# Performance work log

Hardware: AMD Instinct MI355X
Metric: run time of the kernel (lower is better)

## Reference

```python
import jax, jax.numpy as jnp
import numpy as np

N_USERS = 100000
N_ITEMS = 50000
NNZ = 1600000
DIM = 64


def setup_inputs() -> dict:
    key = jax.random.key(0)
    k1, k2, k3, k4, k5, k6, k7 = jax.random.split(key, 7)
    user_x = jax.random.normal(k1, (N_USERS, DIM), dtype=jnp.float32)
    item_x = jax.random.normal(k2, (N_ITEMS, DIM), dtype=jnp.float32)
    # Xavier-uniform-like init for the two weight matrices
    limit = float(np.sqrt(6.0 / (DIM + DIM)))
    user_weight = jax.random.uniform(k3, (DIM, DIM), jnp.float32, -limit, limit)
    item_weight = jax.random.uniform(k4, (DIM, DIM), jnp.float32, -limit, limit)
    # Bipartite adjacency in COO form: ui_graph[r, c] = v ; iu_graph is its transpose
    ui_rows = jax.random.randint(k5, (NNZ,), 0, N_USERS, dtype=jnp.int32)
    ui_cols = jax.random.randint(k6, (NNZ,), 0, N_ITEMS, dtype=jnp.int32)
    ui_vals = jax.random.uniform(k7, (NNZ,), dtype=jnp.float32)
    return {
        "user_x": user_x,
        "item_x": item_x,
        "user_weight": user_weight,
        "item_weight": item_weight,
        "ui_rows": ui_rows,
        "ui_cols": ui_cols,
        "ui_vals": ui_vals,
    }


def _spmm(rows, cols, vals, dense, num_segments):
    # sparse[rows, cols] @ dense  -> gather source rows, scale, scatter-add to dest
    msgs = vals[:, None] * dense[cols]                      # [nnz, d]
    return jax.ops.segment_sum(msgs, rows, num_segments=num_segments)


def reference(user_x, item_x, user_weight, item_weight, ui_rows, ui_cols, ui_vals):
    # dropout p=0.0 -> identity (module default)
    xw_user = user_x @ user_weight                          # [n_users, d]
    xw_item = item_x @ item_weight                          # [n_items, d]
    # out_user = ui_graph @ xw_item ; out_item = iu_graph @ xw_user (iu = ui^T)
    out_user = _spmm(ui_rows, ui_cols, ui_vals, xw_item, N_USERS)
    out_item = _spmm(ui_cols, ui_rows, ui_vals, xw_user, N_ITEMS)
    return jax.nn.relu(out_user), jax.nn.relu(out_item)
```

## Files before the change

### kernel.cpp

```cpp
#include <hip/hip_runtime.h>
#include <hip/hip_bf16.h>

#define N_USERS 100000
#define N_ITEMS 50000
#define NNZ_EDGES 1600000
#define DIM 64

#define BSHIFT_U 7
#define BD_U 128
#define BSHIFT_I 6
#define BD_I 64
#define NBU ((N_USERS + BD_U - 1) / BD_U)
#define NBI ((N_ITEMS + BD_I - 1) / BD_I)
#define NB_MAX 782
#define TILE 4096
#define CAP 2432

#define PREP_GU ((N_USERS + 127) / 128)
#define PREP_GI ((N_ITEMS + 127) / 128)
#define PREP_BIN ((NNZ_EDGES + TILE - 1) / TILE)


__device__ inline unsigned short f32_to_bf16(float f) {
  unsigned u = __float_as_uint(f);
  unsigned r = (u + 0x7FFFu + ((u >> 16) & 1u)) >> 16;
  return (unsigned short)r;
}
__device__ inline float bf16_to_f32(unsigned short h) {
  return __uint_as_float((unsigned)h << 16);
}

__global__ __launch_bounds__(512) void prep_kernel(
    const float* __restrict__ Xu, const float* __restrict__ Wu,
    unsigned short* __restrict__ Yu,
    const float* __restrict__ Xi, const float* __restrict__ Wi,
    unsigned short* __restrict__ Yi,
    const int* __restrict__ rows, const int* __restrict__ cols,
    const float* __restrict__ vals,
    int* __restrict__ cur_u, int* __restrict__ cur_i,
    uint2* __restrict__ out_u, uint2* __restrict__ out_i) {
  __shared__ char smem[49152];
  const int tid = threadIdx.x, lane = tid & 63, wid = tid >> 6;

  if (blockIdx.x < PREP_GU + PREP_GI) {
    float* sW = (float*)smem;
    float* sXTb = (float*)(smem + 16384);
    const int sub = tid >> 8;
    const int stid = tid & 255;

    const float* X; const float* W; unsigned short* Y; int nrows, row_base;
    if (blockIdx.x < PREP_GU) {
      X = Xu; W = Wu; Y = Yu; nrows = N_USERS;
      row_base = blockIdx.x * 128 + sub * 64;
    } else {
      X = Xi; W = Wi; Y = Yi; nrows = N_ITEMS;
      row_base = (blockIdx.x - PREP_GU) * 128 + sub * 64;
    }

    {
      const float4* Wv = (const float4*)W;
      float4* sWv = (float4*)sW;
      #pragma unroll
      for (int i = 0; i < 2; ++i) sWv[tid + i * 512] = Wv[tid + i * 512];
    }
    float* sXT = sXTb + sub * 64 * 64;
    {
      const int r = stid & 63;
      const int k0 = (stid >> 6) * 16;
      const int grow = row_base + r;
      #pragma unroll
      for (int i = 0; i < 4; ++i) {
        float4 v = make_float4(0.f, 0.f, 0.f, 0.f);
        if (grow < nrows) v = ((const float4*)(X + (size_t)grow * DIM + k0))[i];
        sXT[(k0 + i * 4 + 0) * 64 + r] = v.x;
        sXT[(k0 + i * 4 + 1) * 64 + r] = v.y;
        sXT[(k0 + i * 4 + 2) * 64 + r] = v.z;
        sXT[(k0 + i * 4 + 3) * 64 + r] = v.w;
      }
    }
    __syncthreads();

    const int tx = stid & 15;
    const int ty = stid >> 4;
    float acc[4][4] = {{0.f}};

    #pragma unroll 8
    for (int k = 0; k < 64; ++k) {
      const float4 a = *(const float4*)&sXT[k * 64 + ty * 4];
      const float4 b = *(const float4*)&sW[k * 64 + tx * 4];
      acc[0][0] = fmaf(a.x, b.x, acc[0][0]);
      acc[0][1] = fmaf(a.x, b.y, acc[0][1]);
      acc[0][2] = fmaf(a.x, b.z, acc[0][2]);
      acc[0][3] = fmaf(a.x, b.w, acc[0][3]);
      acc[1][0] = fmaf(a.y, b.x, acc[1][0]);
      acc[1][1] = fmaf(a.y, b.y, acc[1][1]);
      acc[1][2] = fmaf(a.y, b.z, acc[1][2]);
      acc[1][3] = fmaf(a.y, b.w, acc[1][3]);
      acc[2][0] = fmaf(a.z, b.x, acc[2][0]);
      acc[2][1] = fmaf(a.z, b.y, acc[2][1]);
      acc[2][2] = fmaf(a.z, b.z, acc[2][2]);
      acc[2][3] = fmaf(a.z, b.w, acc[2][3]);
      acc[3][0] = fmaf(a.w, b.x, acc[3][0]);
      acc[3][1] = fmaf(a.w, b.y, acc[3][1]);
      acc[3][2] = fmaf(a.w, b.z, acc[3][2]);
      acc[3][3] = fmaf(a.w, b.w, acc[3][3]);
    }

    #pragma unroll
    for (int r = 0; r < 4; ++r) {
      const int grow = row_base + ty * 4 + r;
      if (grow < nrows) {
        ushort4 o;
        o.x = f32_to_bf16(acc[r][0]);
        o.y = f32_to_bf16(acc[r][1]);
        o.z = f32_to_bf16(acc[r][2]);
        o.w = f32_to_bf16(acc[r][3]);
        *(ushort4*)(Y + (size_t)grow * DIM + tx * 4) = o;
      }
    }
    return;
  }

  uint2* sbuf = (uint2*)smem;
  unsigned short* sbk = (unsigned short*)(smem + 32768);
  int* sh   = (int*)(smem + 40960);
  int* scnt = (int*)(smem + 44088);
  int* s_w  = (int*)(smem + 47232);

  const int tbase = (blockIdx.x - (PREP_GU + PREP_GI)) * TILE;
  const int total = min(TILE, NNZ_EDGES - tbase);

  int er[8], ec[8]; unsigned ev[8];
  #pragma unroll
  for (int k = 0; k < 8; ++k) {
    const int i = tbase + k * 512 + tid;
    if (i < NNZ_EDGES) {
      er[k] = rows[i];
      ec[k] = cols[i];
      ev[k] = __float_as_uint(vals[i]);
    } else {
      er[k] = -1; ec[k] = 0; ev[k] = 0;
    }
  }

#define BIN_PHASE(BKEXPR, PKEXPR, NB, CUR, OUT)                                \
  {                                                                            \
    for (int j = tid; j < (NB); j += 512) sh[j] = 0;                           \
    __syncthreads();                                                           \
    int bk[8]; unsigned pk[8];                                                 \
    _Pragma("unroll")                                                          \
    for (int k = 0; k < 8; ++k) {                                              \
      if (er[k] >= 0) {                                                        \
        bk[k] = (BKEXPR); pk[k] = (PKEXPR);                                    \
        atomicAdd(&sh[bk[k]], 1);                                              \
      } else { bk[k] = -1; pk[k] = 0; }                                        \
    }                                                                          \
    __syncthreads();                                                           \
    int carry = 0;                                                             \
    for (int cb = 0; cb < (NB); cb += 512) {                                   \
      const int idx = cb + tid;                                                \
      const int x = (idx < (NB)) ? sh[idx] : 0;                                \
      int incl = x;                                                            \
      _Pragma("unroll")                                                        \
      for (int d = 1; d < 64; d <<= 1) {                                       \
        int t = __shfl_up(incl, d);                                            \
        if (lane >= d) incl += t;                                              \
      }                                                                        \
      if (lane == 63) s_w[wid] = incl;                                         \
      __syncthreads();                                                         \
      if (tid == 0) {                                                          \
        int a = 0;                                                             \
        _Pragma("unroll")                                                      \
        for (int w = 0; w < 8; ++w) { const int t = s_w[w]; s_w[w] = a; a += t; } \
        s_w[8] = a;                                                            \
      }                                                                        \
      __syncthreads();                                                         \
      const int excl = carry + s_w[wid] + incl - x;                            \
      if (idx < (NB)) { scnt[idx] = x; sh[idx] = excl; }                       \
      carry += s_w[8];                                                         \
      __syncthreads();                                                         \
    }                                                                          \
    _Pragma("unroll")                                                          \
    for (int k = 0; k < 8; ++k) {                                              \
      if (bk[k] >= 0) {                                                        \
        const int p = atomicAdd(&sh[bk[k]], 1);                                \
        sbuf[p] = make_uint2(pk[k], ev[k]);                                    \
        sbk[p] = (unsigned short)bk[k];                                        \
      }                                                                        \
    }                                                                          \
    __syncthreads();                                                           \
    for (int idx = tid; idx < (NB); idx += 512) {                              \
      const int c = scnt[idx];                                                 \
      const int excl = sh[idx] - c;                                            \
      int g = 0;                                                               \
      if (c > 0) g = atomicAdd(&(CUR)[idx], c);                                \
      scnt[idx] = excl;                                                        \
      sh[idx] = idx * CAP + g;                                                 \
    }                                                                          \
    __syncthreads();                                                           \
    for (int p = tid; p < total; p += 512) {                                   \
      const int b = sbk[p];                                                    \
      (OUT)[sh[b] + (p - scnt[b])] = sbuf[p];                                  \
    }                                                                          \
    __syncthreads();                                                           \
  }

  BIN_PHASE(er[k] >> BSHIFT_U,
            ((unsigned)(er[k] & (BD_U - 1)) << 25) | ((unsigned)ec[k] << 7),
            NBU, cur_u, out_u)
  BIN_PHASE(ec[k] >> BSHIFT_I,
            ((unsigned)(ec[k] & (BD_I - 1)) << 25) | ((unsigned)er[k] << 7),
            NBI, cur_i, out_i)
#undef BIN_PHASE
}

__global__ __launch_bounds__(512) void sort_spmm_kernel(
    const uint2* __restrict__ bin_u, const int* __restrict__ cur_u,
    const unsigned short* __restrict__ xw_item, float* __restrict__ out_user,
    const uint2* __restrict__ bin_i, const int* __restrict__ cur_i,
    const unsigned short* __restrict__ xw_user, float* __restrict__ out_item) {
  __shared__ uint2 sbuf[CAP];
  __shared__ int cnt[128];
  __shared__ int roff[128];
  __shared__ int s_w[2];
  const int tid = threadIdx.x;
  const int lane = tid & 63, wid = tid >> 6;

  const uint2* bin; const int* cur; const unsigned short* xw; float* out;
  int b, bd, ndst;
  if (blockIdx.x < NBU) {
    b = blockIdx.x; bd = BD_U; ndst = N_USERS;
    bin = bin_u; cur = cur_u; xw = xw_item; out = out_user;
  } else {
    b = blockIdx.x - NBU; bd = BD_I; ndst = N_ITEMS;
    bin = bin_i; cur = cur_i; xw = xw_user; out = out_item;
  }
  const int beg = b * CAP;
  const int n = min(cur[b], CAP);

  if (tid < bd) cnt[tid] = 0;
  __syncthreads();

  uint2 rg[5];
  #pragma unroll
  for (int k = 0; k < 5; ++k) {
    const int i = k * 512 + tid;
    if (i < n) {
      rg[k] = bin[beg + i];
      atomicAdd(&cnt[rg[k].x >> 25], 1);
    } else {
      rg[k] = make_uint2(0u, 0u);
    }
  }
  __syncthreads();

  int x = 0, incl = 0;
  if (tid < 128) {
    x = (tid < bd) ? cnt[tid] : 0;
    incl = x;
    #pragma unroll
    for (int d = 1; d < 64; d <<= 1) {
      int t = __shfl_up(incl, d);
      if (lane >= d) incl += t;
    }
    if (lane == 63) s_w[wid] = incl;
  }
  __syncthreads();
  if (tid == 0) {
    const int t0 = s_w[0];
    s_w[0] = 0;
    s_w[1] = t0;
  }
  __syncthreads();
  if (tid < 128) {
    const int excl = s_w[wid] + incl - x;
    if (tid < bd) {
      roff[tid] = excl;
      cnt[tid] = excl;
    }
  }
  __syncthreads();

  #pragma unroll
  for (int k = 0; k < 5; ++k) {
    const int i = k * 512 + tid;
    if (i < n) {
      const int p = atomicAdd(&cnt[rg[k].x >> 25], 1);
      sbuf[p] = rg[k];
    }
  }
  __syncthreads();

  const char* __restrict__ xwb = (const char*)xw + lane * 2;
  for (int r = wid; r < bd; r += 8) {
    const int rb = roff[r], re = cnt[r];
    float acc = 0.f;
    int j = rb;
    for (; j + 16 <= re; j += 16) {
      uint2 e[16];
      #pragma unroll
      for (int q = 0; q < 16; ++q) e[q] = sbuf[j + q];
      unsigned short h[16];
      #pragma unroll
      for (int q = 0; q < 16; ++q)
        h[q] = *(const unsigned short*)(xwb + (e[q].x & 0x01FFFF80u));
      #pragma unroll
      for (int q = 0; q < 16; ++q)
        acc = fmaf(__uint_as_float(e[q].y), bf16_to_f32(h[q]), acc);
    }
    for (; j + 8 <= re; j += 8) {
      uint2 e[8];
      #pragma unroll
      for (int q = 0; q < 8; ++q) e[q] = sbuf[j + q];
      unsigned short h[8];
      #pragma unroll
      for (int q = 0; q < 8; ++q)
        h[q] = *(const unsigned short*)(xwb + (e[q].x & 0x01FFFF80u));
      #pragma unroll
      for (int q = 0; q < 8; ++q)
        acc = fmaf(__uint_as_float(e[q].y), bf16_to_f32(h[q]), acc);
    }
    for (; j + 4 <= re; j += 4) {
      uint2 e[4];
      #pragma unroll
      for (int q = 0; q < 4; ++q) e[q] = sbuf[j + q];
      unsigned short h[4];
      #pragma unroll
      for (int q = 0; q < 4; ++q)
        h[q] = *(const unsigned short*)(xwb + (e[q].x & 0x01FFFF80u));
      #pragma unroll
      for (int q = 0; q < 4; ++q)
        acc = fmaf(__uint_as_float(e[q].y), bf16_to_f32(h[q]), acc);
    }
    for (; j < re; ++j) {
      const uint2 e = sbuf[j];
      acc = fmaf(__uint_as_float(e.y),
                 bf16_to_f32(*(const unsigned short*)(xwb + (e.x & 0x01FFFF80u))),
                 acc);
    }
    const int grow = b * bd + r;
    if (grow < ndst) out[(size_t)grow * DIM + lane] = fmaxf(acc, 0.f);
  }
}

extern "C" void kernel_launch(void* const* d_in, const int* in_sizes, int n_in,
                              void* d_out, int out_size, void* d_ws, size_t ws_size,
                              hipStream_t stream) {
  const float* user_x      = (const float*)d_in[0];
  const float* item_x      = (const float*)d_in[1];
  const float* user_weight = (const float*)d_in[2];
  const float* item_weight = (const float*)d_in[3];
  const int*   ui_rows     = (const int*)d_in[4];
  const int*   ui_cols     = (const int*)d_in[5];
  const float* ui_vals     = (const float*)d_in[6];

  float* out_user = (float*)d_out;
  float* out_item = (float*)d_out + (size_t)N_USERS * DIM;

  unsigned short* xw_user = (unsigned short*)d_ws;
  unsigned short* xw_item = xw_user + (size_t)N_USERS * DIM;
  uint2* binA = (uint2*)(xw_item + (size_t)N_ITEMS * DIM);
  uint2* binB = binA + (size_t)NBU * CAP;
  int*   cur_u = (int*)(binB + (size_t)NBI * CAP);
  int*   cur_i = cur_u + NBU;

  hipMemsetAsync(cur_u, 0, (NBU + NBI) * sizeof(int), stream);

  prep_kernel<<<PREP_GU + PREP_GI + PREP_BIN, 512, 0, stream>>>(
      user_x, user_weight, xw_user, item_x, item_weight, xw_item,
      ui_rows, ui_cols, ui_vals, cur_u, cur_i, binA, binB);

  sort_spmm_kernel<<<NBU + NBI, 512, 0, stream>>>(
      binA, cur_u, xw_item, out_user,
      binB, cur_i, xw_user, out_item);
}
```

Baseline: 110.9 us.

## Gather bf16 rows with 16-byte loads across 8-lane groups and shuffle-reduce

The per-row SpMM gather now splits each wavefront into 8 groups of 8 lanes. Each group processes a different edge, and each lane loads 16 bytes (8 bf16 features) instead of one 2-byte element per lane. Partial sums are combined with xor shuffles and written back as float4 stores. The aim is fewer, wider memory transactions and more edges in flight per wavefront. The cost is eight accumulators per lane, a shuffle reduction, and only one group of lanes doing the stores. Column offsets are now masked once when written into shared memory rather than on every gather.

```diff
diff --git a/kernel.cpp b/kernel.cpp
--- a/kernel.cpp
+++ b/kernel.cpp
@@ -26,9 +26,8 @@
   unsigned r = (u + 0x7FFFu + ((u >> 16) & 1u)) >> 16;
   return (unsigned short)r;
 }
-__device__ inline float bf16_to_f32(unsigned short h) {
-  return __uint_as_float((unsigned)h << 16);
-}
+__device__ inline float bf16_lo(unsigned u) { return __uint_as_float(u << 16); }
+__device__ inline float bf16_hi(unsigned u) { return __uint_as_float(u & 0xFFFF0000u); }
 
 __global__ __launch_bounds__(512) void prep_kernel(
     const float* __restrict__ Xu, const float* __restrict__ Wu,
@@ -238,7 +237,7 @@
   const int beg = b * CAP;
   const int n = min(cur[b], CAP);
 
-  if (tid < bd) cnt[tid] = 0;
+  if (tid < 128) cnt[tid] = 0;
   __syncthreads();
 
   uint2 rg[5];
@@ -286,60 +285,68 @@
     const int i = k * 512 + tid;
     if (i < n) {
       const int p = atomicAdd(&cnt[rg[k].x >> 25], 1);
-      sbuf[p] = rg[k];
-    }
-  }
-  __syncthreads();
-
-  const char* __restrict__ xwb = (const char*)xw + lane * 2;
+      sbuf[p] = make_uint2(rg[k].x & 0x01FFFF80u, rg[k].y);
+    }
+  }
+  __syncthreads();
+
+  const int g = lane >> 3;
+  const int s = lane & 7;
+  const char* __restrict__ xwb = (const char*)xw + s * 16;
+
   for (int r = wid; r < bd; r += 8) {
     const int rb = roff[r], re = cnt[r];
-    float acc = 0.f;
+    float a0 = 0.f, a1 = 0.f, a2 = 0.f, a3 = 0.f;
+    float a4 = 0.f, a5 = 0.f, a6 = 0.f, a7 = 0.f;
+
     int j = rb;
     for (; j + 16 <= re; j += 16) {
-      uint2 e[16];
-      #pragma unroll
-      for (int q = 0; q < 16; ++q) e[q] = sbuf[j + q];
-      unsigned short h[16];
-      #pragma unroll
-      for (int q = 0; q < 16; ++q)
-        h[q] = *(const unsigned short*)(xwb + (e[q].x & 0x01FFFF80u));
-      #pragma unroll
-      for (int q = 0; q < 16; ++q)
-        acc = fmaf(__uint_as_float(e[q].y), bf16_to_f32(h[q]), acc);
-    }
-    for (; j + 8 <= re; j += 8) {
-      uint2 e[8];
-      #pragma unroll
-      for (int q = 0; q < 8; ++q) e[q] = sbuf[j + q];
-      unsigned short h[8];
-      #pragma unroll
-      for (int q = 0; q < 8; ++q)
-        h[q] = *(const unsigned short*)(xwb + (e[q].x & 0x01FFFF80u));
-      #pragma unroll
-      for (int q = 0; q < 8; ++q)
-        acc = fmaf(__uint_as_float(e[q].y), bf16_to_f32(h[q]), acc);
-    }
-    for (; j + 4 <= re; j += 4) {
-      uint2 e[4];
-      #pragma unroll
-      for (int q = 0; q < 4; ++q) e[q] = sbuf[j + q];
-      unsigned short h[4];
-      #pragma unroll
-      for (int q = 0; q < 4; ++q)
-        h[q] = *(const unsigned short*)(xwb + (e[q].x & 0x01FFFF80u));
-      #pragma unroll
-      for (int q = 0; q < 4; ++q)
-        acc = fmaf(__uint_as_float(e[q].y), bf16_to_f32(h[q]), acc);
-    }
-    for (; j < re; ++j) {
-      const uint2 e = sbuf[j];
-      acc = fmaf(__uint_as_float(e.y),
-                 bf16_to_f32(*(const unsigned short*)(xwb + (e.x & 0x01FFFF80u))),
-                 acc);
-    }
+      const uint2 ea = sbuf[j + g];
+      const uint2 eb = sbuf[j + 8 + g];
+      const uint4 ga = *(const uint4*)(xwb + ea.x);
+      const uint4 gb = *(const uint4*)(xwb + eb.x);
+      const float va = __uint_as_float(ea.y);
+      const float vb = __uint_as_float(eb.y);
+      a0 = fmaf(va, bf16_lo(ga.x), a0);  a1 = fmaf(va, bf16_hi(ga.x), a1);
+      a2 = fmaf(va, bf16_lo(ga.y), a2);  a3 = fmaf(va, bf16_hi(ga.y), a3);
+      a4 = fmaf(va, bf16_lo(ga.z), a4);  a5 = fmaf(va, bf16_hi(ga.z), a5);
+      a6 = fmaf(va, bf16_lo(ga.w), a6);  a7 = fmaf(va, bf16_hi(ga.w), a7);
+      a0 = fmaf(vb, bf16_lo(gb.x), a0);  a1 = fmaf(vb, bf16_hi(gb.x), a1);
+      a2 = fmaf(vb, bf16_lo(gb.y), a2);  a3 = fmaf(vb, bf16_hi(gb.y), a3);
+      a4 = fmaf(vb, bf16_lo(gb.z), a4);  a5 = fmaf(vb, bf16_hi(gb.z), a5);
+      a6 = fmaf(vb, bf16_lo(gb.w), a6);  a7 = fmaf(vb, bf16_hi(gb.w), a7);
+    }
+    for (; j < re; j += 8) {
+      const bool valid = (j + g) < re;
+      uint2 e = make_uint2(0u, 0u);
+      if (valid) e = sbuf[j + g];
+      const uint4 gv = *(const uint4*)(xwb + e.x);
+      const float v = valid ? __uint_as_float(e.y) : 0.f;
+      a0 = fmaf(v, bf16_lo(gv.x), a0);  a1 = fmaf(v, bf16_hi(gv.x), a1);
+      a2 = fmaf(v, bf16_lo(gv.y), a2);  a3 = fmaf(v, bf16_hi(gv.y), a3);
+      a4 = fmaf(v, bf16_lo(gv.z), a4);  a5 = fmaf(v, bf16_hi(gv.z), a5);
+      a6 = fmaf(v, bf16_lo(gv.w), a6);  a7 = fmaf(v, bf16_hi(gv.w), a7);
+    }
+
+    #pragma unroll
+    for (int d = 8; d < 64; d <<= 1) {
+      a0 += __shfl_xor(a0, d);  a1 += __shfl_xor(a1, d);
+      a2 += __shfl_xor(a2, d);  a3 += __shfl_xor(a3, d);
+      a4 += __shfl_xor(a4, d);  a5 += __shfl_xor(a5, d);
+      a6 += __shfl_xor(a6, d);  a7 += __shfl_xor(a7, d);
+    }
+
     const int grow = b * bd + r;
-    if (grow < ndst) out[(size_t)grow * DIM + lane] = fmaxf(acc, 0.f);
+    if (g == 0 && grow < ndst) {
+      float4 o0, o1;
+      o0.x = fmaxf(a0, 0.f); o0.y = fmaxf(a1, 0.f);
+      o0.z = fmaxf(a2, 0.f); o0.w = fmaxf(a3, 0.f);
+      o1.x = fmaxf(a4, 0.f); o1.y = fmaxf(a5, 0.f);
+      o1.z = fmaxf(a6, 0.f); o1.w = fmaxf(a7, 0.f);
+      float* op = out + (size_t)grow * DIM + s * 8;
+      *(float4*)op = o0;
+      *(float4*)(op + 4) = o1;
+    }
   }
 }
 
```

New measurement: 111.8 us. Within noise of the previous version (+0.8%).
